# Performance work log

Measured on AMD Instinct MI355X. Metric: run time of the kernel, lower is better.

## Reference

```python
import jax, jax.numpy as jnp
import numpy as np

K, M, N = 8, 1024, 1024  # bits, in_features, out_features (nf)
B_, S_ = 4, 2048

def setup_inputs() -> dict:
    key = jax.random.key(0)
    k1, k2, k3, k4 = jax.random.split(key, 4)
    x = jax.random.normal(k1, (B_, S_, M), dtype=jnp.float32)
    # per-bit +/-1 sign matrices, stored as float (module casts int8 -> x.dtype)
    binary = jnp.where(jax.random.normal(k2, (K, M, N)) > 0, 1.0, -1.0).astype(jnp.float32)
    # positive per-bit, per-output-channel scales (sup decomposition yields positives)
    scale = jax.random.uniform(k3, (K, 1, N), dtype=jnp.float32, minval=0.01, maxval=1.0)
    bias = jax.random.normal(k4, (N,), dtype=jnp.float32)
    return {"x": x, "binary": binary, "scale": scale, "bias": bias}

def reference(x, binary, scale, bias):
    size_out = x.shape[:-1] + (N,)
    x2 = x.reshape(-1, x.shape[-1])                 # [T, m]
    # k separate dense matmuls against +/-1 matrices: [k, T, n]
    xk = jnp.einsum('tm,kmn->ktn', x2, binary)
    out = jnp.sum(xk * scale, axis=0)               # per-bit scale then sum over bits
    out = out + bias
    return out.reshape(size_out)
```

## Files before the change

### kernel.cpp

```cpp
#include <hip/hip_runtime.h>
#include <cstdint>

#define TDIM 8192
#define MDIM 1024
#define NDIM 1024
#define KBITS 8

typedef __bf16 bf16x8 __attribute__((ext_vector_type(8)));
typedef float f32x4 __attribute__((ext_vector_type(4)));

#define GAS(p) ((__attribute__((address_space(1))) void*)(uintptr_t)(p))
#define LAS(p) ((__attribute__((address_space(3))) void*)(uintptr_t)(p))

__device__ __forceinline__ unsigned short f2bf(float f) {
    union { float f; unsigned u; } v; v.f = f;
    unsigned r = v.u + 0x7fffu + ((v.u >> 16) & 1u);
    return (unsigned short)(r >> 16);
}

__global__ __launch_bounds__(256) void prep_x_kernel(const float* __restrict__ x,
                                                     unsigned short* __restrict__ xb) {
    size_t idx = ((size_t)blockIdx.x * 256 + threadIdx.x) * 8;
    float4 a = *(const float4*)(x + idx);
    float4 b = *(const float4*)(x + idx + 4);
    uint4 o;
    o.x = (unsigned)f2bf(a.x) | ((unsigned)f2bf(a.y) << 16);
    o.y = (unsigned)f2bf(a.z) | ((unsigned)f2bf(a.w) << 16);
    o.z = (unsigned)f2bf(b.x) | ((unsigned)f2bf(b.y) << 16);
    o.w = (unsigned)f2bf(b.z) | ((unsigned)f2bf(b.w) << 16);
    *(uint4*)(xb + idx) = o;
}

__global__ __launch_bounds__(256) void prep_w_kernel(const float* __restrict__ binary,
                                                     const float* __restrict__ scale,
                                                     unsigned short* __restrict__ wtr) {
    __shared__ float tile[64][65];
    const int tid = threadIdx.x;
    const int n0 = blockIdx.x * 64;
    const int m0 = blockIdx.y * 64;
    float acc[16];
#pragma unroll
    for (int i = 0; i < 16; ++i) acc[i] = 0.f;
    for (int k = 0; k < KBITS; ++k) {
        const float* bk = binary + ((size_t)k * MDIM + m0) * NDIM + n0;
        const float* sk = scale + (size_t)k * NDIM + n0;
#pragma unroll
        for (int i = 0; i < 16; ++i) {
            int e = tid + i * 256;
            int r = e >> 6, c = e & 63;
            acc[i] += sk[c] * bk[(size_t)r * NDIM + c];
        }
    }
#pragma unroll
    for (int i = 0; i < 16; ++i) {
        int e = tid + i * 256;
        tile[e & 63][e >> 6] = acc[i];
    }
    __syncthreads();
#pragma unroll
    for (int i = 0; i < 16; ++i) {
        int e = tid + i * 256;
        int rn = e >> 6, cm = e & 63;
        wtr[(size_t)(n0 + rn) * MDIM + m0 + cm] = f2bf(tile[rn][cm]);
    }
}

__global__ __launch_bounds__(256) void gemm_kernel(const unsigned short* __restrict__ xb,
                                                   const unsigned short* __restrict__ wtr,
                                                   const float* __restrict__ bias,
                                                   float* __restrict__ out) {
    __shared__ __attribute__((aligned(16))) unsigned short sA[128 * 32];
    __shared__ __attribute__((aligned(16))) unsigned short sB[128 * 32];

    const int tid = threadIdx.x;
    const int lane = tid & 63;
    const int wv = tid >> 6;
    const int wrow = wv >> 1;
    const int wcol = wv & 1;
    const int lrow = lane & 15;
    const int q = lane >> 4;

    const int n0 = blockIdx.x * 128;
    const int t0 = blockIdx.y * 128;

    const int s1 = tid, s2 = tid + 256;
    const int r1 = s1 >> 2, g1 = (s1 & 3) ^ (r1 & 3);
    const int r2 = s2 >> 2, g2 = (s2 & 3) ^ (r2 & 3);

    const unsigned short* a1 = xb + (size_t)(t0 + r1) * MDIM + g1 * 8;
    const unsigned short* a2 = xb + (size_t)(t0 + r2) * MDIM + g2 * 8;
    const unsigned short* b1 = wtr + (size_t)(n0 + r1) * MDIM + g1 * 8;
    const unsigned short* b2 = wtr + (size_t)(n0 + r2) * MDIM + g2 * 8;
    unsigned short* da1 = sA + s1 * 8;
    unsigned short* da2 = sA + s2 * 8;
    unsigned short* db1 = sB + s1 * 8;
    unsigned short* db2 = sB + s2 * 8;

    int a_off[4], b_off[4];
#pragma unroll
    for (int i = 0; i < 4; ++i) {
        int m = wrow * 64 + i * 16 + lrow;
        a_off[i] = (m * 4 + (q ^ (m & 3))) * 8;
        int n = wcol * 64 + i * 16 + lrow;
        b_off[i] = (n * 4 + (q ^ (n & 3))) * 8;
    }

    f32x4 acc[4][4];
    const f32x4 zero = {0.f, 0.f, 0.f, 0.f};
#pragma unroll
    for (int i = 0; i < 4; ++i)
#pragma unroll
        for (int j = 0; j < 4; ++j) acc[i][j] = zero;

    for (int k0 = 0; k0 < MDIM; k0 += 32) {
        __builtin_amdgcn_global_load_lds(GAS(a1 + k0), LAS(da1), 16, 0, 0);
        __builtin_amdgcn_global_load_lds(GAS(a2 + k0), LAS(da2), 16, 0, 0);
        __builtin_amdgcn_global_load_lds(GAS(b1 + k0), LAS(db1), 16, 0, 0);
        __builtin_amdgcn_global_load_lds(GAS(b2 + k0), LAS(db2), 16, 0, 0);
        __syncthreads();

        bf16x8 af[4], bfr[4];
#pragma unroll
        for (int i = 0; i < 4; ++i) af[i] = *(const bf16x8*)(sA + a_off[i]);
#pragma unroll
        for (int i = 0; i < 4; ++i) bfr[i] = *(const bf16x8*)(sB + b_off[i]);

#pragma unroll
        for (int i = 0; i < 4; ++i)
#pragma unroll
            for (int j = 0; j < 4; ++j)
                acc[i][j] = __builtin_amdgcn_mfma_f32_16x16x32_bf16(af[i], bfr[j],
                                                                    acc[i][j], 0, 0, 0);
        __syncthreads();
    }

#pragma unroll
    for (int j = 0; j < 4; ++j) {
        const int n = n0 + wcol * 64 + j * 16 + lrow;
        const float bv = bias[n];
#pragma unroll
        for (int i = 0; i < 4; ++i) {
            const int tb = t0 + wrow * 64 + i * 16 + q * 4;
#pragma unroll
            for (int r = 0; r < 4; ++r) {
                out[(size_t)(tb + r) * NDIM + n] = acc[i][j][r] + bv;
            }
        }
    }
}

extern "C" void kernel_launch(void* const* d_in, const int* in_sizes, int n_in,
                              void* d_out, int out_size, void* d_ws, size_t ws_size,
                              hipStream_t stream) {
    const float* x      = (const float*)d_in[0];
    const float* binary = (const float*)d_in[1];
    const float* scale  = (const float*)d_in[2];
    const float* bias   = (const float*)d_in[3];
    float* out = (float*)d_out;

    unsigned short* xb  = (unsigned short*)d_ws;
    unsigned short* wtr = xb + (size_t)TDIM * MDIM;

    prep_x_kernel<<<(TDIM * MDIM) / (256 * 8), 256, 0, stream>>>(x, xb);
    prep_w_kernel<<<dim3(NDIM / 64, MDIM / 64), 256, 0, stream>>>(binary, scale, wtr);
    gemm_kernel<<<dim3(NDIM / 128, TDIM / 128), 256, 0, stream>>>(xb, wtr, bias, out);
}
```

Before: 153.0 us.

## Merge prep kernels, vectorize weight prep, double GEMM K-tile, swap grid order

Combines the x-to-bf16 conversion and the scaled-weight collapse into a single launch, and vectorizes the weight-prep loads and stores with f32x4/ushort4 accesses. The GEMM K-tile grows from 32 to 64 with an 8-way XOR swizzle and two MFMA half-steps per tile, halving the number of barrier pairs per output tile. The grid is also transposed so consecutive blocks walk along T, which changes how weight tiles are reused in cache. LDS use doubles and the loads are still not overlapped with compute.

```diff
diff --git a/kernel.cpp b/kernel.cpp
--- a/kernel.cpp
+++ b/kernel.cpp
@@ -5,6 +5,7 @@
 #define MDIM 1024
 #define NDIM 1024
 #define KBITS 8
+#define BK 64
 
 typedef __bf16 bf16x8 __attribute__((ext_vector_type(8)));
 typedef float f32x4 __attribute__((ext_vector_type(4)));
@@ -18,59 +19,64 @@
     return (unsigned short)(r >> 16);
 }
 
-__global__ __launch_bounds__(256) void prep_x_kernel(const float* __restrict__ x,
-                                                     unsigned short* __restrict__ xb) {
-    size_t idx = ((size_t)blockIdx.x * 256 + threadIdx.x) * 8;
-    float4 a = *(const float4*)(x + idx);
-    float4 b = *(const float4*)(x + idx + 4);
-    uint4 o;
-    o.x = (unsigned)f2bf(a.x) | ((unsigned)f2bf(a.y) << 16);
-    o.y = (unsigned)f2bf(a.z) | ((unsigned)f2bf(a.w) << 16);
-    o.z = (unsigned)f2bf(b.x) | ((unsigned)f2bf(b.y) << 16);
-    o.w = (unsigned)f2bf(b.z) | ((unsigned)f2bf(b.w) << 16);
-    *(uint4*)(xb + idx) = o;
-}
-
-__global__ __launch_bounds__(256) void prep_w_kernel(const float* __restrict__ binary,
-                                                     const float* __restrict__ scale,
-                                                     unsigned short* __restrict__ wtr) {
+__global__ __launch_bounds__(256) void prep_kernel(const float* __restrict__ x,
+                                                   unsigned short* __restrict__ xb,
+                                                   const float* __restrict__ binary,
+                                                   const float* __restrict__ scale,
+                                                   unsigned short* __restrict__ wtr) {
     __shared__ float tile[64][65];
     const int tid = threadIdx.x;
-    const int n0 = blockIdx.x * 64;
-    const int m0 = blockIdx.y * 64;
-    float acc[16];
+    if (blockIdx.x < 4096) {
+        size_t idx = ((size_t)blockIdx.x * 256 + tid) * 8;
+        float4 a = *(const float4*)(x + idx);
+        float4 b = *(const float4*)(x + idx + 4);
+        uint4 o;
+        o.x = (unsigned)f2bf(a.x) | ((unsigned)f2bf(a.y) << 16);
+        o.y = (unsigned)f2bf(a.z) | ((unsigned)f2bf(a.w) << 16);
+        o.z = (unsigned)f2bf(b.x) | ((unsigned)f2bf(b.y) << 16);
+        o.w = (unsigned)f2bf(b.z) | ((unsigned)f2bf(b.w) << 16);
+        *(uint4*)(xb + idx) = o;
+        return;
+    }
+    const int b2 = blockIdx.x - 4096;
+    const int n0 = (b2 & 15) * 64;
+    const int m0 = (b2 >> 4) * 64;
+    const int r = tid >> 2;
+    const int sub = tid & 3;
+    f32x4 acc4[4];
 #pragma unroll
-    for (int i = 0; i < 16; ++i) acc[i] = 0.f;
+    for (int j = 0; j < 4; ++j) acc4[j] = (f32x4){0.f, 0.f, 0.f, 0.f};
     for (int k = 0; k < KBITS; ++k) {
-        const float* bk = binary + ((size_t)k * MDIM + m0) * NDIM + n0;
-        const float* sk = scale + (size_t)k * NDIM + n0;
+        const float* bk = binary + ((size_t)k * MDIM + m0 + r) * NDIM + n0 + sub * 16;
+        const float* sk = scale + (size_t)k * NDIM + n0 + sub * 16;
 #pragma unroll
-        for (int i = 0; i < 16; ++i) {
-            int e = tid + i * 256;
-            int r = e >> 6, c = e & 63;
-            acc[i] += sk[c] * bk[(size_t)r * NDIM + c];
+        for (int j = 0; j < 4; ++j) {
+            f32x4 v = *(const f32x4*)(bk + j * 4);
+            f32x4 s = *(const f32x4*)(sk + j * 4);
+            acc4[j] += v * s;
         }
     }
 #pragma unroll
-    for (int i = 0; i < 16; ++i) {
-        int e = tid + i * 256;
-        tile[e & 63][e >> 6] = acc[i];
-    }
+    for (int j = 0; j < 4; ++j)
+#pragma unroll
+        for (int e = 0; e < 4; ++e) tile[sub * 16 + j * 4 + e][r] = acc4[j][e];
     __syncthreads();
+    const int rn = tid >> 2;
+    const int cs = (tid & 3) * 16;
+    unsigned short ob[16];
 #pragma unroll
-    for (int i = 0; i < 16; ++i) {
-        int e = tid + i * 256;
-        int rn = e >> 6, cm = e & 63;
-        wtr[(size_t)(n0 + rn) * MDIM + m0 + cm] = f2bf(tile[rn][cm]);
-    }
+    for (int e = 0; e < 16; ++e) ob[e] = f2bf(tile[rn][cs + e]);
+    unsigned short* dst = wtr + (size_t)(n0 + rn) * MDIM + m0 + cs;
+#pragma unroll
+    for (int j = 0; j < 4; ++j) *(ushort4*)(dst + j * 4) = *(ushort4*)(ob + j * 4);
 }
 
 __global__ __launch_bounds__(256) void gemm_kernel(const unsigned short* __restrict__ xb,
                                                    const unsigned short* __restrict__ wtr,
                                                    const float* __restrict__ bias,
                                                    float* __restrict__ out) {
-    __shared__ __attribute__((aligned(16))) unsigned short sA[128 * 32];
-    __shared__ __attribute__((aligned(16))) unsigned short sB[128 * 32];
+    __shared__ __attribute__((aligned(16))) unsigned short sA[128 * BK];
+    __shared__ __attribute__((aligned(16))) unsigned short sB[128 * BK];
 
     const int tid = threadIdx.x;
     const int lane = tid & 63;
@@ -80,30 +86,34 @@
     const int lrow = lane & 15;
     const int q = lane >> 4;
 
-    const int n0 = blockIdx.x * 128;
-    const int t0 = blockIdx.y * 128;
+    const int t0 = blockIdx.x * 128;
+    const int n0 = blockIdx.y * 128;
 
-    const int s1 = tid, s2 = tid + 256;
-    const int r1 = s1 >> 2, g1 = (s1 & 3) ^ (r1 & 3);
-    const int r2 = s2 >> 2, g2 = (s2 & 3) ^ (r2 & 3);
+    const unsigned short* srcA[4];
+    const unsigned short* srcB[4];
+    unsigned short* dstA[4];
+    unsigned short* dstB[4];
+#pragma unroll
+    for (int j = 0; j < 4; ++j) {
+        int s = tid + j * 256;
+        int r = s >> 3;
+        int g = (s & 7) ^ (r & 7);
+        srcA[j] = xb + (size_t)(t0 + r) * MDIM + g * 8;
+        srcB[j] = wtr + (size_t)(n0 + r) * MDIM + g * 8;
+        dstA[j] = sA + s * 8;
+        dstB[j] = sB + s * 8;
+    }
 
-    const unsigned short* a1 = xb + (size_t)(t0 + r1) * MDIM + g1 * 8;
-    const unsigned short* a2 = xb + (size_t)(t0 + r2) * MDIM + g2 * 8;
-    const unsigned short* b1 = wtr + (size_t)(n0 + r1) * MDIM + g1 * 8;
-    const unsigned short* b2 = wtr + (size_t)(n0 + r2) * MDIM + g2 * 8;
-    unsigned short* da1 = sA + s1 * 8;
-    unsigned short* da2 = sA + s2 * 8;
-    unsigned short* db1 = sB + s1 * 8;
-    unsigned short* db2 = sB + s2 * 8;
-
-    int a_off[4], b_off[4];
+    int a_off[2][4], b_off[2][4];
 #pragma unroll
-    for (int i = 0; i < 4; ++i) {
-        int m = wrow * 64 + i * 16 + lrow;
-        a_off[i] = (m * 4 + (q ^ (m & 3))) * 8;
-        int n = wcol * 64 + i * 16 + lrow;
-        b_off[i] = (n * 4 + (q ^ (n & 3))) * 8;
-    }
+    for (int h = 0; h < 2; ++h)
+#pragma unroll
+        for (int i = 0; i < 4; ++i) {
+            int m = wrow * 64 + i * 16 + lrow;
+            a_off[h][i] = (m * 8 + ((h * 4 + q) ^ (m & 7))) * 8;
+            int n = wcol * 64 + i * 16 + lrow;
+            b_off[h][i] = (n * 8 + ((h * 4 + q) ^ (n & 7))) * 8;
+        }
 
     f32x4 acc[4][4];
     const f32x4 zero = {0.f, 0.f, 0.f, 0.f};
@@ -112,25 +122,29 @@
 #pragma unroll
         for (int j = 0; j < 4; ++j) acc[i][j] = zero;
 
-    for (int k0 = 0; k0 < MDIM; k0 += 32) {
-        __builtin_amdgcn_global_load_lds(GAS(a1 + k0), LAS(da1), 16, 0, 0);
-        __builtin_amdgcn_global_load_lds(GAS(a2 + k0), LAS(da2), 16, 0, 0);
-        __builtin_amdgcn_global_load_lds(GAS(b1 + k0), LAS(db1), 16, 0, 0);
-        __builtin_amdgcn_global_load_lds(GAS(b2 + k0), LAS(db2), 16, 0, 0);
+    for (int k0 = 0; k0 < MDIM; k0 += BK) {
+#pragma unroll
+        for (int j = 0; j < 4; ++j)
+            __builtin_amdgcn_global_load_lds(GAS(srcA[j] + k0), LAS(dstA[j]), 16, 0, 0);
+#pragma unroll
+        for (int j = 0; j < 4; ++j)
+            __builtin_amdgcn_global_load_lds(GAS(srcB[j] + k0), LAS(dstB[j]), 16, 0, 0);
         __syncthreads();
 
-        bf16x8 af[4], bfr[4];
 #pragma unroll
-        for (int i = 0; i < 4; ++i) af[i] = *(const bf16x8*)(sA + a_off[i]);
+        for (int h = 0; h < 2; ++h) {
+            bf16x8 af[4], bfr[4];
 #pragma unroll
-        for (int i = 0; i < 4; ++i) bfr[i] = *(const bf16x8*)(sB + b_off[i]);
-
+            for (int i = 0; i < 4; ++i) af[i] = *(const bf16x8*)(sA + a_off[h][i]);
 #pragma unroll
-        for (int i = 0; i < 4; ++i)
+            for (int i = 0; i < 4; ++i) bfr[i] = *(const bf16x8*)(sB + b_off[h][i]);
 #pragma unroll
-            for (int j = 0; j < 4; ++j)
-                acc[i][j] = __builtin_amdgcn_mfma_f32_16x16x32_bf16(af[i], bfr[j],
-                                                                    acc[i][j], 0, 0, 0);
+            for (int i = 0; i < 4; ++i)
+#pragma unroll
+                for (int j = 0; j < 4; ++j)
+                    acc[i][j] = __builtin_amdgcn_mfma_f32_16x16x32_bf16(af[i], bfr[j],
+                                                                        acc[i][j], 0, 0, 0);
+        }
         __syncthreads();
     }
 
@@ -161,7 +175,6 @@
     unsigned short* xb  = (unsigned short*)d_ws;
     unsigned short* wtr = xb + (size_t)TDIM * MDIM;
 
-    prep_x_kernel<<<(TDIM * MDIM) / (256 * 8), 256, 0, stream>>>(x, xb);
-    prep_w_kernel<<<dim3(NDIM / 64, MDIM / 64), 256, 0, stream>>>(binary, scale, wtr);
-    gemm_kernel<<<dim3(NDIM / 128, TDIM / 128), 256, 0, stream>>>(xb, wtr, bias, out);
+    prep_kernel<<<4096 + 256, 256, 0, stream>>>(x, xb, binary, scale, wtr);
+    gemm_kernel<<<dim3(TDIM / 128, NDIM / 128), 256, 0, stream>>>(xb, wtr, bias, out);
 }
```

After: 151.7 us. No clear change (-0.9%).
